# Kernel optimization log

Hardware: AMD Instinct MI355X
Metric: run time of the kernel (lower is better)

The kernel has to match this reference:

```python
import jax, jax.numpy as jnp
import numpy as np

ALPHA = 0.2  # leaky relu slope
NEG = -9e15


def setup_inputs() -> dict:
    key = jax.random.key(0)
    k1, k2, k3, k4 = jax.random.split(key, 4)
    B, N, Fin, Fout = 16, 2048, 256, 256
    h = jax.random.normal(k1, (B, N, Fin), dtype=jnp.float32)
    adj = jax.random.randint(k2, (B, N, N), 0, 2, dtype=jnp.int32)
    # xavier_uniform with gain 1.414 on [B, Fin, Fout] (fan over last two dims)
    limW = 1.414 * np.sqrt(6.0 / (Fin + Fout))
    W = jax.random.uniform(k3, (B, Fin, Fout), minval=-limW, maxval=limW, dtype=jnp.float32)
    lima = 1.414 * np.sqrt(6.0 / (2 * Fout + 1))
    a = jax.random.uniform(k4, (B, 2 * Fout, 1), minval=-lima, maxval=lima, dtype=jnp.float32)
    return {"h": h, "adj": adj, "W": W, "a": a}


def reference(h, adj, W, a):
    Fout = W.shape[-1]
    Wh = jnp.einsum('bnf,bfo->bno', h, W)                 # [B,N,Fout]
    Wh1 = jnp.einsum('bno,bo->bn', Wh, a[:, :Fout, 0])    # [B,N]
    Wh2 = jnp.einsum('bno,bo->bn', Wh, a[:, Fout:, 0])    # [B,N]
    e = Wh1[:, :, None] + Wh2[:, None, :]                 # [B,N,N]
    e = jnp.where(e > 0, e, ALPHA * e)                    # leaky relu
    att = jnp.where(adj > 0, e, NEG)
    att = jax.nn.softmax(att, axis=1)                     # NOTE: dim=1 as in source
    # dropout: eval mode -> identity
    h_prime = jnp.einsum('bij,bjo->bio', att, Wh)         # [B,N,Fout]
    return jax.nn.elu(h_prime)                            # concat=True
```

## Files before the change

### kernel.cpp

```cpp
#include <hip/hip_runtime.h>
#include <hip/hip_bf16.h>

typedef unsigned short u16;
typedef unsigned long long u64;
typedef __attribute__((ext_vector_type(8))) short bf16x8;
typedef __attribute__((ext_vector_type(4))) float f32x4;

#define NB 16
#define NN 2048
#define FF 256
#define LOG2E 1.4426950408889634f

__device__ __forceinline__ u16 f2bf(float x) {
    union { float f; unsigned u; } v; v.f = x;
    unsigned r = v.u + 0x7fffu + ((v.u >> 16) & 1u);
    return (u16)(r >> 16);
}

#define GLD_LDS(g, l) __builtin_amdgcn_global_load_lds((const __attribute__((address_space(1))) void*)(g), (__attribute__((address_space(3))) void*)(l), 16, 0, 0)

__global__ __launch_bounds__(256) void k_prep_w(const float* __restrict__ W, const float* __restrict__ a,
                                                u16* __restrict__ WT, float* __restrict__ u1, float* __restrict__ u2) {
    int b = blockIdx.y, t = threadIdx.x;
    __shared__ float a1s[FF], a2s[FF];
    a1s[t] = a[b*2*FF + t];
    a2s[t] = a[b*2*FF + FF + t];
    __syncthreads();
    int f = blockIdx.x*64 + (t >> 2);
    int o0 = (t & 3) * 64;
    const float* wrow = W + (size_t)(b*FF + f)*FF + o0;
    u16* wtb = WT + (size_t)b*FF*FF;
    float s1 = 0.f, s2 = 0.f;
#pragma unroll
    for (int c = 0; c < 16; ++c) {
        float4 v = *(const float4*)(wrow + c*4);
        int o = o0 + c*4;
        s1 += v.x*a1s[o] + v.y*a1s[o+1] + v.z*a1s[o+2] + v.w*a1s[o+3];
        s2 += v.x*a2s[o] + v.y*a2s[o+1] + v.z*a2s[o+2] + v.w*a2s[o+3];
        wtb[(size_t)(o+0)*FF + f] = f2bf(v.x);
        wtb[(size_t)(o+1)*FF + f] = f2bf(v.y);
        wtb[(size_t)(o+2)*FF + f] = f2bf(v.z);
        wtb[(size_t)(o+3)*FF + f] = f2bf(v.w);
    }
    s1 += __shfl_xor(s1, 1); s1 += __shfl_xor(s1, 2);
    s2 += __shfl_xor(s2, 1); s2 += __shfl_xor(s2, 2);
    if ((t & 3) == 0) { u1[b*FF + f] = s1; u2[b*FF + f] = s2; }
}

__global__ __launch_bounds__(256) void k_wh(const float* __restrict__ h, const u16* __restrict__ WT,
                                            const float* __restrict__ u1, const float* __restrict__ u2,
                                            u16* __restrict__ WhT, float* __restrict__ Wh1, float* __restrict__ Wh2) {
    int bid = blockIdx.x;
    int nid = (bid & 7)*64 + (bid >> 3);
    int b  = nid >> 5;
    int i0 = (nid & 31) * 64;
    int t = threadIdx.x, lane = t & 63, wave = t >> 6;
    __shared__ alignas(16) u16 At[256*64];
    __shared__ alignas(16) u16 Bt[64*64];
    __shared__ float u1s[FF], u2s[FF];
    u1s[t] = u1[b*FF + t];
    u2s[t] = u2[b*FF + t];

    const u16*   WTb = WT + (size_t)b*FF*FF;
    const float* hb  = h + ((size_t)b*NN + i0)*FF;
    int r = t >> 2, q = t & 3, kq = q*16;

    f32x4 acc[4][4];
#pragma unroll
    for (int x = 0; x < 4; ++x)
#pragma unroll
        for (int y = 0; y < 4; ++y) acc[x][y] = (f32x4)0.f;
    float s1 = 0.f, s2 = 0.f;
    __syncthreads();

#pragma unroll 1
    for (int kk = 0; kk < 4; ++kk) {
        int k0 = kk*64;
#pragma unroll
        for (int is = 0; is < 8; ++is) {
            int s = is*256 + t;
            int row = s >> 3, jbp = s & 7;
            int jbl = jbp ^ (row & 7);
            GLD_LDS(WTb + (size_t)row*FF + k0 + jbl*8, &At[s*8]);
        }
        {
            const float* hp = hb + (size_t)r*FF + k0 + kq;
            float4 f0 = *(const float4*)(hp + 0);
            float4 f1 = *(const float4*)(hp + 4);
            float4 f2 = *(const float4*)(hp + 8);
            float4 f3 = *(const float4*)(hp + 12);
            float fv[16] = {f0.x,f0.y,f0.z,f0.w, f1.x,f1.y,f1.z,f1.w,
                            f2.x,f2.y,f2.z,f2.w, f3.x,f3.y,f3.z,f3.w};
            union { u16 u[16]; bf16x8 v[2]; } cv;
#pragma unroll
            for (int e = 0; e < 16; ++e) {
                int kidx = k0 + kq + e;
                s1 += fv[e]*u1s[kidx];
                s2 += fv[e]*u2s[kidx];
                cv.u[e] = f2bf(fv[e]);
            }
            int rx = r & 7;
            *(bf16x8*)&Bt[r*64 + ((q*2 + 0) ^ rx)*8] = cv.v[0];
            *(bf16x8*)&Bt[r*64 + ((q*2 + 1) ^ rx)*8] = cv.v[1];
        }
        __syncthreads();
#pragma unroll
        for (int kc = 0; kc < 2; ++kc) {
            int jl = kc*4 + (lane >> 4);
            bf16x8 af[4], bfr[4];
#pragma unroll
            for (int mi = 0; mi < 4; ++mi) {
                int rr2 = wave*64 + mi*16 + (lane & 15);
                af[mi] = *(const bf16x8*)&At[rr2*64 + ((jl ^ (rr2 & 7))*8)];
            }
#pragma unroll
            for (int ni = 0; ni < 4; ++ni) {
                int rr2 = ni*16 + (lane & 15);
                bfr[ni] = *(const bf16x8*)&Bt[rr2*64 + ((jl ^ (rr2 & 7))*8)];
            }
#pragma unroll
            for (int mi = 0; mi < 4; ++mi)
#pragma unroll
                for (int ni = 0; ni < 4; ++ni)
                    acc[mi][ni] = __builtin_amdgcn_mfma_f32_16x16x32_bf16(af[mi], bfr[ni], acc[mi][ni], 0, 0, 0);
        }
        __syncthreads();
    }
    s1 += __shfl_xor(s1, 1); s1 += __shfl_xor(s1, 2);
    s2 += __shfl_xor(s2, 1); s2 += __shfl_xor(s2, 2);
    if (q == 0) { Wh1[b*NN + i0 + r] = s1*LOG2E; Wh2[b*NN + i0 + r] = s2*LOG2E; }

    u16* Wo = WhT + (size_t)b*FF*NN;
#pragma unroll
    for (int mi = 0; mi < 4; ++mi)
#pragma unroll
        for (int ni = 0; ni < 4; ++ni) {
            int i = i0 + ni*16 + (lane & 15);
#pragma unroll
            for (int rr = 0; rr < 4; ++rr) {
                int o = wave*64 + mi*16 + (lane >> 4)*4 + rr;
                Wo[(size_t)o*NN + i] = f2bf(acc[mi][ni][rr]);
            }
        }
}

__global__ __launch_bounds__(256) void k_colsum(const int* __restrict__ adj, const float* __restrict__ Wh1,
                                                const float* __restrict__ Wh2, float* __restrict__ pS,
                                                u64* __restrict__ packed) {
    int b = blockIdx.z, ic = blockIdx.y, jt = blockIdx.x;
    int t = threadIdx.x, lane = t & 63, wave = t >> 6;
    __shared__ float wh1s[256];
    int ibase = ic*256;
    wh1s[t] = Wh1[b*NN + ibase + t];
    __syncthreads();
    int j = jt*256 + wave*16 + (lane & 15) + (lane >> 4)*64;
    float wh2j = Wh2[b*NN + j];
    const int* acol = adj + (size_t)b*NN*NN + (size_t)ibase*NN + j;
    u64* prow = packed + ((size_t)(b*NN + ibase))*32 + wave*8 + jt;
    float s = 0.f;
#pragma unroll 1
    for (int ii = 0; ii < 256; ii += 8) {
        int v[8];
#pragma unroll
        for (int rr = 0; rr < 8; ++rr) v[rr] = acol[(size_t)(ii + rr)*NN];
#pragma unroll
        for (int rr = 0; rr < 8; ++rr) {
            bool p = v[rr] > 0;
            u64 m = __ballot(p);
            if (lane == 0) prow[(size_t)(ii + rr)*32] = m;
            float tt = wh1s[ii + rr] + wh2j;
            float lr = fmaxf(tt, 0.2f*tt);
            float e = __builtin_amdgcn_exp2f(lr);
            s += p ? e : 0.f;
        }
    }
    pS[((size_t)(b*8 + ic))*NN + j] = s;
}

__global__ __launch_bounds__(512, 1) void k_gemm3(const u16* __restrict__ WhT, const u64* __restrict__ packed,
                                                  const float* __restrict__ Wh1, const float* __restrict__ Wh2,
                                                  const float* __restrict__ pS, float* __restrict__ out) {
    int bid = blockIdx.x;
    int nid = (bid & 7)*32 + (bid >> 3);
    int b  = nid >> 4;
    int i0 = (nid & 15) * 128;
    int t = threadIdx.x, lane = t & 63, wave = t >> 6;
    int wm = wave >> 2, wn = wave & 3;
    __shared__ alignas(16) u16 At[2][128*64];
    __shared__ alignas(16) u16 Bt[3][256*64];
    __shared__ float wh2s[NN];
    __shared__ float e2ps[NN];
    __shared__ float e2ns[NN];
    __shared__ unsigned zlut[4];

    const u16* Wo = WhT + (size_t)b*FF*NN;
    int rA = t >> 2, qA = t & 3;
    const u64* pkrow = packed + ((size_t)b*NN + i0 + rA)*32 + qA*8;

    float wh1r = Wh1[b*NN + i0 + rA];
    float e1p = __builtin_amdgcn_exp2f(wh1r);
    float e1n = __builtin_amdgcn_exp2f(0.2f*wh1r);

#pragma unroll
    for (int c = 0; c < 4; ++c) {
        int idx = c*512 + t;
        float w2 = Wh2[b*NN + idx];
        float s = 0.f;
#pragma unroll
        for (int cc = 0; cc < 8; ++cc) s += pS[((size_t)(b*8 + cc))*NN + idx];
        float inv = (s > 0.f) ? 1.0f/s : 0.0f;
        wh2s[idx] = w2;
        e2ps[idx] = __builtin_amdgcn_exp2f(w2) * inv;
        e2ns[idx] = __builtin_amdgcn_exp2f(0.2f*w2) * inv;
    }
    if (t < 4) zlut[t] = ((t & 1) ? 0xFFFFu : 0u) | ((t & 2) ? 0xFFFF0000u : 0u);

    auto stageB = [&](int kk, int bbuf) {
        int k0 = kk*64;
#pragma unroll
        for (int is = 0; is < 4; ++is) {
            int s = is*512 + t;
            int row = s >> 3, jbp = s & 7;
            int jbl = jbp ^ (row & 7);
            GLD_LDS(Wo + (size_t)row*NN + k0 + jbl*8, &Bt[bbuf][s*8]);
        }
    };
    auto genA = [&](int g, int abuf, unsigned mask16) {
        int rx = rA & 7;
#pragma unroll
        for (int hf = 0; hf < 2; ++hf) {
            union { unsigned w[4]; bf16x8 v; } ob;
#pragma unroll
            for (int q4 = 0; q4 < 2; ++q4) {
                int jb = g*64 + qA*16 + hf*8 + q4*4;
                float4 w2 = *(const float4*)&wh2s[jb];
                float4 tp = *(const float4*)&e2ps[jb];
                float4 tn = *(const float4*)&e2ns[jb];
                float xs[4] = {w2.x, w2.y, w2.z, w2.w};
                float ps[4] = {tp.x, tp.y, tp.z, tp.w};
                float ns[4] = {tn.x, tn.y, tn.z, tn.w};
                float pe[4];
#pragma unroll
                for (int e = 0; e < 4; ++e) {
                    float tt = wh1r + xs[e];
                    bool pos = tt > 0.f;
                    pe[e] = (pos ? e1p : e1n) * (pos ? ps[e] : ns[e]);
                }
                unsigned bits = mask16 >> (hf*8 + q4*4);
#pragma unroll
                for (int p = 0; p < 2; ++p) {
                    unsigned w;
                    asm("v_cvt_pk_bf16_f32 %0, %1, %2" : "=v"(w) : "v"(pe[2*p]), "v"(pe[2*p+1]));
                    ob.w[q4*2 + p] = w & zlut[(bits >> (2*p)) & 3];
                }
            }
            *(bf16x8*)&At[abuf][rA*64 + (((qA*2 + hf) ^ rx)*8)] = ob.v;
        }
    };

#define MM(mi, ni, af, bf) acc[mi][ni] = __builtin_amdgcn_mfma_f32_16x16x32_bf16(af, bf, acc[mi][ni], 0, 0, 0)

    f32x4 acc[4][4];
#pragma unroll
    for (int x = 0; x < 4; ++x)
#pragma unroll
        for (int y = 0; y < 4; ++y) acc[x][y] = (f32x4)0.f;

    u64 mcur = pkrow[0];
    u64 mnext = pkrow[1];
    __syncthreads();
    stageB(0, 0);
    stageB(1, 1);
    genA(0, 0, (unsigned)(mcur & 0xffffu));
    asm volatile("s_waitcnt vmcnt(4) lgkmcnt(0)" ::: "memory");
    __builtin_amdgcn_s_barrier();

    int ibr = 0, ibs = 2;
#pragma unroll 1
    for (int kk = 0; kk < 32; ++kk) {
        int g = kk + 1;
        if (g < 32 && (g & 3) == 0) {
            mcur = mnext;
            if (g + 4 < 32) mnext = pkrow[(g + 4) >> 2];
        }
        if (kk + 2 < 32) stageB(kk + 2, ibs);
        if (g < 32) {
            unsigned mask16 = (unsigned)((mcur >> ((g & 3)*16)) & 0xffffu);
            genA(g, g & 1, mask16);
        }
        int ra = kk & 1;
#pragma unroll
        for (int kc = 0; kc < 2; ++kc) {
            int jl = kc*4 + (lane >> 4);
            bf16x8 af[2], af2[2], bfr[4];
#pragma unroll
            for (int mi = 0; mi < 2; ++mi) {
                int rr2 = wm*64 + mi*16 + (lane & 15);
                af[mi] = *(const bf16x8*)&At[ra][rr2*64 + ((jl ^ (rr2 & 7))*8)];
            }
#pragma unroll
            for (int ni = 0; ni < 4; ++ni) {
                int rr2 = wn*64 + ni*16 + (lane & 15);
                bfr[ni] = *(const bf16x8*)&Bt[ibr][rr2*64 + ((jl ^ (rr2 & 7))*8)];
            }
            __builtin_amdgcn_s_setprio(1);
            MM(0,0,af[0],bfr[0]); MM(0,1,af[0],bfr[1]); MM(0,2,af[0],bfr[2]); MM(0,3,af[0],bfr[3]);
            MM(1,0,af[1],bfr[0]); MM(1,1,af[1],bfr[1]); MM(1,2,af[1],bfr[2]); MM(1,3,af[1],bfr[3]);
            __builtin_amdgcn_s_setprio(0);
#pragma unroll
            for (int mi = 2; mi < 4; ++mi) {
                int rr2 = wm*64 + mi*16 + (lane & 15);
                af2[mi-2] = *(const bf16x8*)&At[ra][rr2*64 + ((jl ^ (rr2 & 7))*8)];
            }
            __builtin_amdgcn_s_setprio(1);
            MM(2,0,af2[0],bfr[0]); MM(2,1,af2[0],bfr[1]); MM(2,2,af2[0],bfr[2]); MM(2,3,af2[0],bfr[3]);
            MM(3,0,af2[1],bfr[0]); MM(3,1,af2[1],bfr[1]); MM(3,2,af2[1],bfr[2]); MM(3,3,af2[1],bfr[3]);
            __builtin_amdgcn_s_setprio(0);
        }
        if (kk < 30) asm volatile("s_waitcnt vmcnt(4) lgkmcnt(0)" ::: "memory");
        else         asm volatile("s_waitcnt vmcnt(0) lgkmcnt(0)" ::: "memory");
        __builtin_amdgcn_s_barrier();
        ibr = (ibr + 1 == 3) ? 0 : ibr + 1;
        ibs = (ibs + 1 == 3) ? 0 : ibs + 1;
    }
#undef MM

    float* ob2 = out + ((size_t)b*NN)*FF;
#pragma unroll
    for (int mi = 0; mi < 4; ++mi)
#pragma unroll
        for (int ni = 0; ni < 4; ++ni) {
            int o = wn*64 + ni*16 + (lane & 15);
#pragma unroll
            for (int rr = 0; rr < 4; ++rr) {
                int i = i0 + wm*64 + mi*16 + (lane >> 4)*4 + rr;
                float x = acc[mi][ni][rr];
                float y = (x > 0.f) ? x : (__builtin_amdgcn_exp2f(x*LOG2E) - 1.f);
                ob2[(size_t)i*FF + o] = y;
            }
        }
}

extern "C" void kernel_launch(void* const* d_in, const int* in_sizes, int n_in,
                              void* d_out, int out_size, void* d_ws, size_t ws_size,
                              hipStream_t stream) {
    const float* h   = (const float*)d_in[0];
    const int*   adj = (const int*)d_in[1];
    const float* W   = (const float*)d_in[2];
    const float* a   = (const float*)d_in[3];
    float* out = (float*)d_out;

    char* w = (char*)d_ws;
    const size_t MB = 1u << 20;
    u16* WT   = (u16*)(w + 0);
    u16* WhT  = (u16*)(w + 2*MB);
    u64* packed = (u64*)(w + 18*MB);
    float* pS  = (float*)(w + 26*MB);
    float* Wh1 = (float*)(w + 27*MB);
    float* Wh2 = (float*)(w + 27*MB + 131072);
    float* u1  = (float*)(w + 27*MB + 2*131072);
    float* u2  = (float*)(w + 27*MB + 2*131072 + 16384);

    k_prep_w<<<dim3(4, 16), 256, 0, stream>>>(W, a, WT, u1, u2);
    k_wh<<<dim3(512), 256, 0, stream>>>(h, WT, u1, u2, WhT, Wh1, Wh2);
    k_colsum<<<dim3(8, 8, 16), 256, 0, stream>>>(adj, Wh1, Wh2, pS, packed);
    k_gemm3<<<dim3(256), 512, 0, stream>>>(WhT, packed, Wh1, Wh2, pS, out);
}
```

Baseline: 158.0 us.

## Split attention GEMM over output columns and pack LDS tables to bf16

The final aggregation GEMM now tiles the output feature dimension into two 128-wide halves. This doubles the grid to 512 blocks, halves the accumulators and B tile per block, and lets more blocks share a CU (launch bounds 512,4). The per-column softmax tables (Wh2, exp terms times inverse column sum) are stored in LDS as packed bf16 to cut LDS footprint and read traffic. B staging drops from triple to double buffering. The cost is that each block regenerates the full attention A tile, so the exp/mask work is doubled overall. Rounding Wh2 and the exp factors to bf16 also adds precision loss, including in the sign test of the leaky-relu branch.

```diff
diff --git a/kernel.cpp b/kernel.cpp
--- a/kernel.cpp
+++ b/kernel.cpp
@@ -177,23 +177,24 @@
     pS[((size_t)(b*8 + ic))*NN + j] = s;
 }
 
-__global__ __launch_bounds__(512, 1) void k_gemm3(const u16* __restrict__ WhT, const u64* __restrict__ packed,
+__global__ __launch_bounds__(512, 4) void k_gemm3(const u16* __restrict__ WhT, const u64* __restrict__ packed,
                                                   const float* __restrict__ Wh1, const float* __restrict__ Wh2,
                                                   const float* __restrict__ pS, float* __restrict__ out) {
     int bid = blockIdx.x;
-    int nid = (bid & 7)*32 + (bid >> 3);
-    int b  = nid >> 4;
-    int i0 = (nid & 15) * 128;
+    int nid = (bid & 7)*64 + (bid >> 3);
+    int b   = nid >> 5;
+    int rem = nid & 31;
+    int i0  = (rem >> 1) * 128;
+    int o0  = (rem & 1) * 128;
     int t = threadIdx.x, lane = t & 63, wave = t >> 6;
     int wm = wave >> 2, wn = wave & 3;
     __shared__ alignas(16) u16 At[2][128*64];
-    __shared__ alignas(16) u16 Bt[3][256*64];
-    __shared__ float wh2s[NN];
-    __shared__ float e2ps[NN];
-    __shared__ float e2ns[NN];
+    __shared__ alignas(16) u16 Bt[2][128*64];
+    __shared__ unsigned eps2[NN];
+    __shared__ u16 wh2b[NN];
     __shared__ unsigned zlut[4];
 
-    const u16* Wo = WhT + (size_t)b*FF*NN;
+    const u16* Wo = WhT + (size_t)b*FF*NN + (size_t)o0*NN;
     int rA = t >> 2, qA = t & 3;
     const u64* pkrow = packed + ((size_t)b*NN + i0 + rA)*32 + qA*8;
 
@@ -209,16 +210,17 @@
 #pragma unroll
         for (int cc = 0; cc < 8; ++cc) s += pS[((size_t)(b*8 + cc))*NN + idx];
         float inv = (s > 0.f) ? 1.0f/s : 0.0f;
-        wh2s[idx] = w2;
-        e2ps[idx] = __builtin_amdgcn_exp2f(w2) * inv;
-        e2ns[idx] = __builtin_amdgcn_exp2f(0.2f*w2) * inv;
+        u16 ep = f2bf(__builtin_amdgcn_exp2f(w2) * inv);
+        u16 en = f2bf(__builtin_amdgcn_exp2f(0.2f*w2) * inv);
+        eps2[idx] = ((unsigned)ep << 16) | (unsigned)en;
+        wh2b[idx] = f2bf(w2);
     }
     if (t < 4) zlut[t] = ((t & 1) ? 0xFFFFu : 0u) | ((t & 2) ? 0xFFFF0000u : 0u);
 
-    auto stageB = [&](int kk, int bbuf) {
-        int k0 = kk*64;
-#pragma unroll
-        for (int is = 0; is < 4; ++is) {
+    auto stageB = [&](int kkk, int bbuf) {
+        int k0 = kkk*64;
+#pragma unroll
+        for (int is = 0; is < 2; ++is) {
             int s = is*512 + t;
             int row = s >> 3, jbp = s & 7;
             int jbl = jbp ^ (row & 7);
@@ -229,30 +231,29 @@
         int rx = rA & 7;
 #pragma unroll
         for (int hf = 0; hf < 2; ++hf) {
+            unsigned mhf = (mask16 >> (hf*8)) & 0xffu;
+            int jb = g*64 + qA*16 + hf*8;
+            uint4 w2q = *(const uint4*)&wh2b[jb];
+            uint4 ea  = *(const uint4*)&eps2[jb];
+            uint4 eb  = *(const uint4*)&eps2[jb + 4];
+            unsigned wp[4] = {w2q.x, w2q.y, w2q.z, w2q.w};
+            unsigned ew[8] = {ea.x, ea.y, ea.z, ea.w, eb.x, eb.y, eb.z, eb.w};
+            float pe[8];
+#pragma unroll
+            for (int e = 0; e < 8; ++e) {
+                union { unsigned u; float f; } wf;
+                wf.u = (e & 1) ? (wp[e >> 1] & 0xFFFF0000u) : (wp[e >> 1] << 16);
+                bool pos = (wh1r + wf.f) > 0.f;
+                union { unsigned u; float f; } ef;
+                ef.u = pos ? (ew[e] & 0xFFFF0000u) : (ew[e] << 16);
+                pe[e] = (pos ? e1p : e1n) * ef.f;
+            }
             union { unsigned w[4]; bf16x8 v; } ob;
 #pragma unroll
-            for (int q4 = 0; q4 < 2; ++q4) {
-                int jb = g*64 + qA*16 + hf*8 + q4*4;
-                float4 w2 = *(const float4*)&wh2s[jb];
-                float4 tp = *(const float4*)&e2ps[jb];
-                float4 tn = *(const float4*)&e2ns[jb];
-                float xs[4] = {w2.x, w2.y, w2.z, w2.w};
-                float ps[4] = {tp.x, tp.y, tp.z, tp.w};
-                float ns[4] = {tn.x, tn.y, tn.z, tn.w};
-                float pe[4];
-#pragma unroll
-                for (int e = 0; e < 4; ++e) {
-                    float tt = wh1r + xs[e];
-                    bool pos = tt > 0.f;
-                    pe[e] = (pos ? e1p : e1n) * (pos ? ps[e] : ns[e]);
-                }
-                unsigned bits = mask16 >> (hf*8 + q4*4);
-#pragma unroll
-                for (int p = 0; p < 2; ++p) {
-                    unsigned w;
-                    asm("v_cvt_pk_bf16_f32 %0, %1, %2" : "=v"(w) : "v"(pe[2*p]), "v"(pe[2*p+1]));
-                    ob.w[q4*2 + p] = w & zlut[(bits >> (2*p)) & 3];
-                }
+            for (int p = 0; p < 4; ++p) {
+                unsigned wv;
+                asm("v_cvt_pk_bf16_f32 %0, %1, %2" : "=v"(wv) : "v"(pe[2*p]), "v"(pe[2*p+1]));
+                ob.w[p] = wv & zlut[(mhf >> (2*p)) & 3];
             }
             *(bf16x8*)&At[abuf][rA*64 + (((qA*2 + hf) ^ rx)*8)] = ob.v;
         }
@@ -260,68 +261,57 @@
 
 #define MM(mi, ni, af, bf) acc[mi][ni] = __builtin_amdgcn_mfma_f32_16x16x32_bf16(af, bf, acc[mi][ni], 0, 0, 0)
 
-    f32x4 acc[4][4];
+    f32x4 acc[4][2];
 #pragma unroll
     for (int x = 0; x < 4; ++x)
 #pragma unroll
-        for (int y = 0; y < 4; ++y) acc[x][y] = (f32x4)0.f;
+        for (int y = 0; y < 2; ++y) acc[x][y] = (f32x4)0.f;
 
     u64 mcur = pkrow[0];
     u64 mnext = pkrow[1];
     __syncthreads();
     stageB(0, 0);
-    stageB(1, 1);
     genA(0, 0, (unsigned)(mcur & 0xffffu));
-    asm volatile("s_waitcnt vmcnt(4) lgkmcnt(0)" ::: "memory");
+    asm volatile("s_waitcnt lgkmcnt(0)" ::: "memory");
     __builtin_amdgcn_s_barrier();
 
-    int ibr = 0, ibs = 2;
 #pragma unroll 1
     for (int kk = 0; kk < 32; ++kk) {
+        int cur = kk & 1;
         int g = kk + 1;
-        if (g < 32 && (g & 3) == 0) {
-            mcur = mnext;
-            if (g + 4 < 32) mnext = pkrow[(g + 4) >> 2];
-        }
-        if (kk + 2 < 32) stageB(kk + 2, ibs);
         if (g < 32) {
-            unsigned mask16 = (unsigned)((mcur >> ((g & 3)*16)) & 0xffffu);
-            genA(g, g & 1, mask16);
-        }
-        int ra = kk & 1;
+            if ((g & 3) == 0) {
+                mcur = mnext;
+                if (g + 4 < 32) mnext = pkrow[(g + 4) >> 2];
+            }
+            stageB(g, cur ^ 1);
+            genA(g, cur ^ 1, (unsigned)((mcur >> ((g & 3)*16)) & 0xffffu));
+        }
+        if (kk < 31) asm volatile("s_waitcnt vmcnt(2)" ::: "memory");
+        else         asm volatile("s_waitcnt vmcnt(0)" ::: "memory");
 #pragma unroll
         for (int kc = 0; kc < 2; ++kc) {
             int jl = kc*4 + (lane >> 4);
-            bf16x8 af[2], af2[2], bfr[4];
-#pragma unroll
-            for (int mi = 0; mi < 2; ++mi) {
-                int rr2 = wm*64 + mi*16 + (lane & 15);
-                af[mi] = *(const bf16x8*)&At[ra][rr2*64 + ((jl ^ (rr2 & 7))*8)];
-            }
-#pragma unroll
-            for (int ni = 0; ni < 4; ++ni) {
-                int rr2 = wn*64 + ni*16 + (lane & 15);
-                bfr[ni] = *(const bf16x8*)&Bt[ibr][rr2*64 + ((jl ^ (rr2 & 7))*8)];
+            bf16x8 af[4], bfr[2];
+#pragma unroll
+            for (int mi = 0; mi < 4; ++mi) {
+                int r2 = wm*64 + mi*16 + (lane & 15);
+                af[mi] = *(const bf16x8*)&At[cur][r2*64 + ((jl ^ (r2 & 7))*8)];
+            }
+#pragma unroll
+            for (int ni = 0; ni < 2; ++ni) {
+                int r2 = wn*32 + ni*16 + (lane & 15);
+                bfr[ni] = *(const bf16x8*)&Bt[cur][r2*64 + ((jl ^ (r2 & 7))*8)];
             }
             __builtin_amdgcn_s_setprio(1);
-            MM(0,0,af[0],bfr[0]); MM(0,1,af[0],bfr[1]); MM(0,2,af[0],bfr[2]); MM(0,3,af[0],bfr[3]);
-            MM(1,0,af[1],bfr[0]); MM(1,1,af[1],bfr[1]); MM(1,2,af[1],bfr[2]); MM(1,3,af[1],bfr[3]);
+            MM(0,0,af[0],bfr[0]); MM(0,1,af[0],bfr[1]);
+            MM(1,0,af[1],bfr[0]); MM(1,1,af[1],bfr[1]);
+            MM(2,0,af[2],bfr[0]); MM(2,1,af[2],bfr[1]);
+            MM(3,0,af[3],bfr[0]); MM(3,1,af[3],bfr[1]);
             __builtin_amdgcn_s_setprio(0);
-#pragma unroll
-            for (int mi = 2; mi < 4; ++mi) {
-                int rr2 = wm*64 + mi*16 + (lane & 15);
-                af2[mi-2] = *(const bf16x8*)&At[ra][rr2*64 + ((jl ^ (rr2 & 7))*8)];
-            }
-            __builtin_amdgcn_s_setprio(1);
-            MM(2,0,af2[0],bfr[0]); MM(2,1,af2[0],bfr[1]); MM(2,2,af2[0],bfr[2]); MM(2,3,af2[0],bfr[3]);
-            MM(3,0,af2[1],bfr[0]); MM(3,1,af2[1],bfr[1]); MM(3,2,af2[1],bfr[2]); MM(3,3,af2[1],bfr[3]);
-            __builtin_amdgcn_s_setprio(0);
-        }
-        if (kk < 30) asm volatile("s_waitcnt vmcnt(4) lgkmcnt(0)" ::: "memory");
-        else         asm volatile("s_waitcnt vmcnt(0) lgkmcnt(0)" ::: "memory");
+        }
+        asm volatile("s_waitcnt lgkmcnt(0)" ::: "memory");
         __builtin_amdgcn_s_barrier();
-        ibr = (ibr + 1 == 3) ? 0 : ibr + 1;
-        ibs = (ibs + 1 == 3) ? 0 : ibs + 1;
     }
 #undef MM
 
@@ -329,8 +319,8 @@
 #pragma unroll
     for (int mi = 0; mi < 4; ++mi)
 #pragma unroll
-        for (int ni = 0; ni < 4; ++ni) {
-            int o = wn*64 + ni*16 + (lane & 15);
+        for (int ni = 0; ni < 2; ++ni) {
+            int o = o0 + wn*32 + ni*16 + (lane & 15);
 #pragma unroll
             for (int rr = 0; rr < 4; ++rr) {
                 int i = i0 + wm*64 + mi*16 + (lane >> 4)*4 + rr;
@@ -364,5 +354,5 @@
     k_prep_w<<<dim3(4, 16), 256, 0, stream>>>(W, a, WT, u1, u2);
     k_wh<<<dim3(512), 256, 0, stream>>>(h, WT, u1, u2, WhT, Wh1, Wh2);
     k_colsum<<<dim3(8, 8, 16), 256, 0, stream>>>(adj, Wh1, Wh2, pS, packed);
-    k_gemm3<<<dim3(256), 512, 0, stream>>>(WhT, packed, Wh1, Wh2, pS, out);
-}
+    k_gemm3<<<dim3(512), 512, 0, stream>>>(WhT, packed, Wh1, Wh2, pS, out);
+}
```

Measured after the change: 164.3 us. 1.04x slower.
